# Kernel optimization log

Hardware: AMD Instinct MI355X
Metric: run time of the kernel (lower is better)

Reference implementation:

```python
import jax, jax.numpy as jnp
import numpy as np

M = 4          # num_models
B = 128        # per-model batch
C = 10         # num_classes
K = 32         # num_centroids
F = 512        # feature_dimension
NZ = 512       # noise_dimension
H = 512        # hidden_dimension
SIGMA = 1.0    # length_scale (not learnable)


def be_fc(x, W, r, s, b=None):
    # BatchEnsemble (Ensemble_orderFC): x is [M*N, in], rows ordered by model.
    N = x.shape[0] // M
    xm = x.reshape(M, N, -1) * r[:, None, :]
    out = jnp.einsum('mni,io->mno', xm, W) * s[:, None, :]
    if b is not None:
        out = out + b[:, None, :]
    return out.reshape(M * N, -1)


def setup_inputs() -> dict:
    key = jax.random.key(0)
    ks = jax.random.split(key, 16)
    sc = lambda fan_in: 1.0 / np.sqrt(fan_in)
    inp = {
        'x': jax.random.normal(ks[0], (M * B, F), dtype=jnp.float32),
        'proto_noise': jax.random.normal(ks[1], (C * K, NZ), dtype=jnp.float32),
        # layer_W: F -> F*C, bias=False
        'W_lw': jax.random.normal(ks[2], (F, F * C), dtype=jnp.float32) * sc(F),
        'r_lw': 1.0 + 0.1 * jax.random.normal(ks[3], (M, F), dtype=jnp.float32),
        's_lw': 1.0 + 0.1 * jax.random.normal(ks[4], (M, F * C), dtype=jnp.float32),
        # fc1_p: (C + NZ) -> H
        'W1': jax.random.normal(ks[5], (C + NZ, H), dtype=jnp.float32) * sc(C + NZ),
        'r1': 1.0 + 0.1 * jax.random.normal(ks[6], (M, C + NZ), dtype=jnp.float32),
        's1': 1.0 + 0.1 * jax.random.normal(ks[7], (M, H), dtype=jnp.float32),
        'b1': jnp.zeros((M, H), dtype=jnp.float32),
        # fc2_p: H -> F
        'W2': jax.random.normal(ks[8], (H, F), dtype=jnp.float32) * sc(H),
        'r2': 1.0 + 0.1 * jax.random.normal(ks[9], (M, H), dtype=jnp.float32),
        's2': 1.0 + 0.1 * jax.random.normal(ks[10], (M, F), dtype=jnp.float32),
        'b2': jnp.zeros((M, F), dtype=jnp.float32),
    }
    return inp


def reference(x, proto_noise, W_lw, r_lw, s_lw, W1, r1, s1, b1, W2, r2, s2, b2):
    # ---- get_prototype ----
    onehot = jnp.repeat(jnp.eye(C, dtype=x.dtype), K, axis=0)        # [C*K, C]
    proto_in = jnp.concatenate([proto_noise, onehot], axis=1)        # [C*K, NZ+C]
    proto_in = jnp.tile(proto_in, (M, 1))                            # [M*C*K, NZ+C]
    h = jax.nn.relu(be_fc(proto_in, W1, r1, s1, b1))
    proto = be_fc(h, W2, r2, s2, b2).reshape(M, C, K, F)

    # ---- last_layer ----
    z = be_fc(x, W_lw, r_lw, s_lw)                                   # [M*B, F*C]
    z = z.reshape(M * B, F, C)

    # ---- output_layer: broadcast RBF squared-distance reduction ----
    zt = jnp.transpose(z.reshape(M, B, F, C), (0, 1, 3, 2))          # [M, B, C, F]
    diff = zt[:, :, :, None, :] - proto[:, None, :, :, :]            # [M, B, C, K, F]
    distances = -(diff ** 2).mean(axis=(-1, -2)) / (2.0 * SIGMA ** 2)  # [M, B, C]

    logit = distances.reshape(-1, C)                                 # [M*B, C]
    return jnp.exp(logit)
```

## Files before the change

### kernel.cpp

```cpp
#include <hip/hip_runtime.h>
#include <math.h>

#define MM 4
#define BB 128
#define CC 10
#define KK 32
#define FF 512
#define HH 512
#define NP 320
#define OUTW 5120

using bf16x8 = __attribute__((ext_vector_type(8))) short;
using f32x4  = __attribute__((ext_vector_type(4))) float;

__device__ __forceinline__ unsigned short f2bf(float f) {
    unsigned int u = __float_as_uint(f);
    u += 0x7FFFu + ((u >> 16) & 1u);
    return (unsigned short)(u >> 16);
}

template<int EPI, int ASRC, int BSRC, int WR, int WC, int I, int J,
         int KSTEPS, int KREALB, int RPM, int NCOLS>
__device__ __forceinline__ void gemm_tile(
    const int bx, const int by,
    const unsigned short* __restrict__ Abf, const float* __restrict__ Af32,
    const float* __restrict__ ascale,
    const unsigned short* __restrict__ Btbf, const float* __restrict__ Bf32,
    const float* __restrict__ s, const float* __restrict__ bias,
    const float* __restrict__ auxr, void* __restrict__ outv,
    float* __restrict__ auxw, unsigned short* smem)
{
    constexpr int TR = WR * I * 16;
    constexpr int TC = WC * J * 16;
    constexpr int BUFE = (TR + TC) * 32;
    const int t = threadIdx.x;
    const int lane = t & 63;
    const int w = t >> 6;
    const int wr = w / WC, wc = w % WC;
    const int l15 = lane & 15, l4 = lane >> 4;
    const int rowT = by * TR, colT = bx * TC;
    const int m = rowT / RPM;

    constexpr bool AGUARD = (TR * 4 < 256);
    const bool aact = !AGUARD || (t < TR * 4);
    const int asrow = t >> 2, ag = t & 3;
    const int stA = asrow * 32 + ((ag ^ ((asrow >> 1) & 3)) * 8);
    const unsigned short* gA = nullptr;
    const float* gAf = nullptr;
    const float* scp = nullptr;
    int cn = 0;
    if constexpr (ASRC == 0) {
        if (aact) gA = Abf + (size_t)(rowT + asrow) * 512 + ag * 8;
    } else {
        gAf = Af32 + (size_t)((rowT % NP) + asrow) * 512 + ag * 8;
        scp = ascale + (size_t)m * 522 + ag * 8;
        cn = ((rowT % NP) + asrow) >> 5;
    }
    const int bsrow = t >> 2, bg = t & 3;
    const int stB0 = bsrow * 32 + ((bg ^ ((bsrow >> 1) & 3)) * 8);
    const int bcol = t & 63, bkg = t >> 6;
    const int stB1 = bcol * 32 + ((bkg ^ ((bcol >> 1) & 3)) * 8);
    const unsigned short* gB = nullptr;
    if constexpr (BSRC == 0)
        gB = Btbf + (size_t)(colT + bsrow) * 512 + bg * 8;

    int offA[I], offB[J];
#pragma unroll
    for (int i = 0; i < I; ++i) {
        int rA = wr * (I * 16) + i * 16 + l15;
        offA[i] = rA * 32 + ((l4 ^ ((rA >> 1) & 3)) * 8);
    }
#pragma unroll
    for (int j = 0; j < J; ++j) {
        int rB = wc * (J * 16) + j * 16 + l15;
        offB[j] = rB * 32 + ((l4 ^ ((rB >> 1) & 3)) * 8);
    }

    f32x4 acc[I][J];
#pragma unroll
    for (int i = 0; i < I; ++i)
#pragma unroll
        for (int j = 0; j < J; ++j) acc[i][j] = (f32x4){0.f, 0.f, 0.f, 0.f};

    uint4 ra, rb;
    float4 nf0, nf1, ns0, ns1;
    float rbf[8];

#define FETCH(KS)                                                              \
    {                                                                          \
        const int k0 = (KS) * 32;                                              \
        if constexpr (ASRC == 0) {                                             \
            if (aact) ra = *(const uint4*)(gA + k0);                           \
        } else {                                                               \
            if (k0 < 512) {                                                    \
                nf0 = *(const float4*)(gAf + k0);                              \
                nf1 = *(const float4*)(gAf + k0 + 4);                          \
                ns0 = *(const float4*)(scp + k0);                              \
                ns1 = *(const float4*)(scp + k0 + 4);                          \
            }                                                                  \
        }                                                                      \
        if constexpr (BSRC == 0) {                                             \
            rb = *(const uint4*)(gB + k0);                                     \
        } else {                                                               \
            _Pragma("unroll")                                                  \
            for (int q = 0; q < 8; ++q) {                                      \
                int gk = k0 + bkg * 8 + q;                                     \
                rbf[q] = (gk < KREALB)                                         \
                    ? Bf32[(size_t)gk * NCOLS + colT + bcol] : 0.f;            \
            }                                                                  \
        }                                                                      \
    }

#define WRITE(KS, BUF)                                                         \
    {                                                                          \
        const int k0 = (KS) * 32;                                              \
        unsigned short* As_ = smem + (BUF) * BUFE;                             \
        unsigned short* Bs_ = As_ + TR * 32;                                   \
        if constexpr (ASRC == 0) {                                             \
            if (aact) *(uint4*)(As_ + stA) = ra;                               \
        } else {                                                               \
            union { unsigned short u[8]; uint4 q; } o;                         \
            if (k0 < 512) {                                                    \
                float vv[8] = {nf0.x, nf0.y, nf0.z, nf0.w,                     \
                               nf1.x, nf1.y, nf1.z, nf1.w};                    \
                float ss[8] = {ns0.x, ns0.y, ns0.z, ns0.w,                     \
                               ns1.x, ns1.y, ns1.z, ns1.w};                    \
                _Pragma("unroll")                                              \
                for (int q = 0; q < 8; ++q) o.u[q] = f2bf(vv[q] * ss[q]);      \
            } else {                                                           \
                _Pragma("unroll")                                              \
                for (int q = 0; q < 8; ++q) {                                  \
                    int gk = k0 + ag * 8 + q;                                  \
                    float v = (gk < 522 && (gk - 512) == cn)                   \
                        ? ascale[(size_t)m * 522 + gk] : 0.f;                  \
                    o.u[q] = f2bf(v);                                          \
                }                                                              \
            }                                                                  \
            *(uint4*)(As_ + stA) = o.q;                                        \
        }                                                                      \
        if constexpr (BSRC == 0) {                                             \
            *(uint4*)(Bs_ + stB0) = rb;                                        \
        } else {                                                               \
            union { unsigned short u[8]; uint4 q; } o;                         \
            _Pragma("unroll")                                                  \
            for (int q = 0; q < 8; ++q) o.u[q] = f2bf(rbf[q]);                 \
            *(uint4*)(Bs_ + stB1) = o.q;                                       \
        }                                                                      \
    }

    FETCH(0);
    WRITE(0, 0);
    __syncthreads();

#pragma unroll 1
    for (int ks = 0; ks < KSTEPS; ++ks) {
        const int cur = ks & 1;
        if (ks + 1 < KSTEPS) FETCH(ks + 1);
        const unsigned short* As_ = smem + cur * BUFE;
        const unsigned short* Bs_ = As_ + TR * 32;
        bf16x8 af[I], bfv[J];
#pragma unroll
        for (int i = 0; i < I; ++i) af[i] = *(const bf16x8*)(As_ + offA[i]);
#pragma unroll
        for (int j = 0; j < J; ++j) bfv[j] = *(const bf16x8*)(Bs_ + offB[j]);
#pragma unroll
        for (int i = 0; i < I; ++i)
#pragma unroll
            for (int j = 0; j < J; ++j)
                acc[i][j] = __builtin_amdgcn_mfma_f32_16x16x32_bf16(
                    af[i], bfv[j], acc[i][j], 0, 0, 0);
        if (ks + 1 < KSTEPS) {
            WRITE(ks + 1, cur ^ 1);
            __syncthreads();
        }
    }
#undef FETCH
#undef WRITE

    if constexpr (EPI == 0) {
#pragma unroll
        for (int j = 0; j < J; ++j) {
            const int col = colT + wc * (J * 16) + j * 16 + l15;
            const float sv = s[(size_t)m * NCOLS + col];
            const float bv = bias[(size_t)m * NCOLS + col];
            const float rv = auxr[(size_t)m * NCOLS + col];
#pragma unroll
            for (int i = 0; i < I; ++i)
#pragma unroll
                for (int ir = 0; ir < 4; ++ir) {
                    const int row = rowT + wr * (I * 16) + i * 16 + l4 * 4 + ir;
                    float v = fmaxf(acc[i][j][ir] * sv + bv, 0.f) * rv;
                    ((unsigned short*)outv)[(size_t)row * NCOLS + col] = f2bf(v);
                }
        }
    } else if constexpr (EPI == 1) {
        static_assert(WR == 1 && I == 2 && J == 1, "EPI1 geometry");
        const int mq = rowT / NP;
        const int c = (rowT % NP) / KK;
        const int mc = mq * CC + c;
        const int col = colT + wc * 16 + l15;
        const float sv = s[(size_t)mq * NCOLS + col];
        const float bv = bias[(size_t)mq * NCOLS + col];
        float cs = 0.f, sq = 0.f;
#pragma unroll
        for (int i = 0; i < I; ++i)
#pragma unroll
            for (int ir = 0; ir < 4; ++ir) {
                float v = acc[i][0][ir] * sv + bv;
                cs += v;
                sq += v * v;
            }
        cs += __shfl_xor(cs, 16, 64);
        cs += __shfl_xor(cs, 32, 64);
        if (l4 == 0) ((float*)outv)[(size_t)mc * FF + col] = cs;
#pragma unroll
        for (int off = 1; off < 64; off <<= 1) sq += __shfl_xor(sq, off, 64);
        if (lane == 0) auxw[mc * 32 + bx * 4 + w] = sq;
    } else {
        static_assert(WR == 2 && WC == 2 && I == 2 && J == 2, "EPI2 geometry");
        const int cb = colT >> 9;
        const int slot = ((bx & 7) << 1) | wc;
        float sv[J], pv[J];
#pragma unroll
        for (int j = 0; j < J; ++j) {
            const int col = colT + wc * (J * 16) + j * 16 + l15;
            sv[j] = s[(size_t)m * NCOLS + (col & 511) * 10 + (col >> 9)];
            pv[j] = bias[(size_t)m * NCOLS + col];
        }
        float* dst = (float*)outv;
#pragma unroll
        for (int i = 0; i < I; ++i)
#pragma unroll
            for (int ir = 0; ir < 4; ++ir) {
                const int row = rowT + wr * (I * 16) + i * 16 + l4 * 4 + ir;
                float znv = 0.f, crv = 0.f;
#pragma unroll
                for (int j = 0; j < J; ++j) {
                    float v = acc[i][j][ir] * sv[j];
                    znv += v * v;
                    crv += v * pv[j];
                }
#pragma unroll
                for (int off = 1; off < 16; off <<= 1) {
                    znv += __shfl_xor(znv, off, 64);
                    crv += __shfl_xor(crv, off, 64);
                }
                if (l15 == 0) {
                    float2 o = {znv, crv};
                    *(float2*)(dst + ((size_t)(row * CC + cb) * 16 + slot) * 2) = o;
                }
            }
    }
}

__global__ __launch_bounds__(256) void k_phase1(
    const float* __restrict__ noise, const float* __restrict__ r1,
    const float* __restrict__ W1, const float* __restrict__ s1,
    const float* __restrict__ b1, const float* __restrict__ r2,
    const float* __restrict__ W_lw, const float* __restrict__ x,
    const float* __restrict__ r_lw,
    unsigned short* __restrict__ A2, unsigned short* __restrict__ Wlwt,
    unsigned short* __restrict__ xr)
{
    __shared__ __align__(16) unsigned short smem[8192];
    const int b = blockIdx.x;
    const int t = threadIdx.x;
    if (b < 160) {
        gemm_tile<0, 2, 1, 2, 2, 2, 2, 17, 522, NP, HH>(
            b % 8, b / 8, nullptr, noise, r1, nullptr, W1,
            s1, b1, r2, (void*)A2, nullptr, smem);
    } else if (b < 800) {
        unsigned short (*T)[65] = (unsigned short (*)[65])smem;
        const int bb = b - 160;
        const int n0 = (bb % 80) * 64, k0 = (bb / 80) * 64;
#pragma unroll
        for (int p = 0; p < 4; ++p) {
            int kk = (t >> 4) + p * 16;
            int nn = (t & 15) * 4;
            float4 v = *(const float4*)(W_lw + (size_t)(k0 + kk) * OUTW + n0 + nn);
            T[nn + 0][kk] = f2bf(v.x);
            T[nn + 1][kk] = f2bf(v.y);
            T[nn + 2][kk] = f2bf(v.z);
            T[nn + 3][kk] = f2bf(v.w);
        }
        __syncthreads();
#pragma unroll
        for (int p = 0; p < 2; ++p) {
            int n = (t >> 3) + p * 32;
            int kg = t & 7;
            union { unsigned short u[8]; uint4 v; } o;
#pragma unroll
            for (int q = 0; q < 8; ++q) o.u[q] = T[n][kg * 8 + q];
            int gn = n0 + n;
            int dr = (gn % 10) * 512 + gn / 10;
            *(uint4*)(Wlwt + (size_t)dr * 512 + k0 + kg * 8) = o.v;
        }
    } else {
        const int id = (b - 800) * 256 + t;
        const int row = id >> 6, g = id & 63;
        const int mq = row >> 7;
        const float* xp = x + (size_t)row * 512 + g * 8;
        const float* rp = r_lw + (size_t)mq * 512 + g * 8;
        union { unsigned short u[8]; uint4 v; } o;
#pragma unroll
        for (int q = 0; q < 8; ++q) o.u[q] = f2bf(xp[q] * rp[q]);
        *(uint4*)(xr + (size_t)row * 512 + g * 8) = o.v;
    }
}

__global__ __launch_bounds__(256) void k_phase2(
    const unsigned short* __restrict__ A2, const float* __restrict__ W2,
    const float* __restrict__ s2, const float* __restrict__ b2,
    float* __restrict__ psum, float* __restrict__ pn_part)
{
    __shared__ __align__(16) unsigned short smem[6144];
    gemm_tile<1, 0, 1, 1, 4, 2, 1, 16, 512, NP, FF>(
        blockIdx.x, blockIdx.y, A2, nullptr, nullptr, nullptr, W2,
        s2, b2, nullptr, (void*)psum, pn_part, smem);
}

__global__ __launch_bounds__(256) void k_phase3(
    const unsigned short* __restrict__ xr, const unsigned short* __restrict__ Wlwt,
    const float* __restrict__ s_lw, const float* __restrict__ psum,
    float* __restrict__ dist_part)
{
    __shared__ __align__(16) unsigned short smem[8192];
    gemm_tile<2, 0, 0, 2, 2, 2, 2, 16, 512, BB, OUTW>(
        blockIdx.x, blockIdx.y, xr, nullptr, nullptr, Wlwt, nullptr,
        s_lw, psum, nullptr, (void*)dist_part, nullptr, smem);
}

__global__ __launch_bounds__(256) void k_out(
    const float* __restrict__ dist_part, const float* __restrict__ pn_part,
    float* __restrict__ out)
{
    const int id = blockIdx.x * 256 + threadIdx.x;
    const int c = id % 10;
    const int mb = id / 10;
    const int mc = (mb >> 7) * 10 + c;
    const float* dp = dist_part + (size_t)id * 32;
    float zn = 0.f, cr = 0.f;
#pragma unroll
    for (int q = 0; q < 16; ++q) {
        zn += dp[q * 2];
        cr += dp[q * 2 + 1];
    }
    float pnv = 0.f;
#pragma unroll
    for (int q = 0; q < 32; ++q) pnv += pn_part[mc * 32 + q];
    const float inv = 1.f / (2.f * (float)KK * (float)FF);
    out[id] = expf(-((float)KK * zn - 2.f * cr + pnv) * inv);
}

extern "C" void kernel_launch(void* const* d_in, const int* in_sizes, int n_in,
                              void* d_out, int out_size, void* d_ws, size_t ws_size,
                              hipStream_t stream) {
    const float* x     = (const float*)d_in[0];
    const float* noise = (const float*)d_in[1];
    const float* W_lw  = (const float*)d_in[2];
    const float* r_lw  = (const float*)d_in[3];
    const float* s_lw  = (const float*)d_in[4];
    const float* W1    = (const float*)d_in[5];
    const float* r1    = (const float*)d_in[6];
    const float* s1    = (const float*)d_in[7];
    const float* b1    = (const float*)d_in[8];
    const float* W2    = (const float*)d_in[9];
    const float* r2    = (const float*)d_in[10];
    const float* s2    = (const float*)d_in[11];
    const float* b2    = (const float*)d_in[12];
    float* out = (float*)d_out;

    char* base = (char*)d_ws;
    float* psum          = (float*)(base + 0);
    float* pn_part       = (float*)(base + 81920);
    float* dist_part     = (float*)(base + 87040);
    unsigned short* A2   = (unsigned short*)(base + 742400);
    unsigned short* xr   = (unsigned short*)(base + 2053120);
    unsigned short* Wlwt = (unsigned short*)(base + 2577408);

    k_phase1<<<928, 256, 0, stream>>>(noise, r1, W1, s1, b1, r2, W_lw, x, r_lw,
                                      A2, Wlwt, xr);
    k_phase2<<<dim3(8, 40), 256, 0, stream>>>(A2, W2, s2, b2, psum, pn_part);
    k_phase3<<<dim3(80, 8), 256, 0, stream>>>(xr, Wlwt, s_lw, psum, dist_part);
    k_out<<<20, 256, 0, stream>>>(dist_part, pn_part, out);
}
```

Baseline: 56.16 us.

## Stage W_lw directly in GEMM, register double-buffer, fuse output reduction via ticket

Drops the separate W_lw transpose/bf16 pre-pass in phase1 and instead loads fp32 W_lw columns directly in phase3's B staging with in-register conversion. Phase3 gets a larger 128-row tile, a two-deep register prefetch, and an epilogue that reorders columns through shared memory to emit per-column-block partials. The separate output kernel is folded into phase3 through an atomic ticket and spin-wait by trailing blocks, which saves a launch. The trade-offs are uncoalesced strided fp32 B loads, and a spin-wait that can deadlock if the waiting blocks become resident before the producer blocks.

```diff
diff --git a/kernel.cpp b/kernel.cpp
--- a/kernel.cpp
+++ b/kernel.cpp
@@ -19,20 +19,22 @@
     return (unsigned short)(u >> 16);
 }
 
-template<int EPI, int ASRC, int BSRC, int WR, int WC, int I, int J,
+template<int EPI, int ASRC, int WR, int WC, int I, int J,
          int KSTEPS, int KREALB, int RPM, int NCOLS>
 __device__ __forceinline__ void gemm_tile(
     const int bx, const int by,
     const unsigned short* __restrict__ Abf, const float* __restrict__ Af32,
-    const float* __restrict__ ascale,
-    const unsigned short* __restrict__ Btbf, const float* __restrict__ Bf32,
+    const float* __restrict__ ascale, const float* __restrict__ Bf32,
     const float* __restrict__ s, const float* __restrict__ bias,
     const float* __restrict__ auxr, void* __restrict__ outv,
     float* __restrict__ auxw, unsigned short* smem)
 {
     constexpr int TR = WR * I * 16;
     constexpr int TC = WC * J * 16;
+    static_assert(TC == 64, "direct B staging needs TC==64");
     constexpr int BUFE = (TR + TC) * 32;
+    constexpr int NUA = (TR * 4 + 255) / 256;
+
     const int t = threadIdx.x;
     const int lane = t & 63;
     const int w = t >> 6;
@@ -41,38 +43,40 @@
     const int rowT = by * TR, colT = bx * TC;
     const int m = rowT / RPM;
 
-    constexpr bool AGUARD = (TR * 4 < 256);
-    const bool aact = !AGUARD || (t < TR * 4);
-    const int asrow = t >> 2, ag = t & 3;
-    const int stA = asrow * 32 + ((ag ^ ((asrow >> 1) & 3)) * 8);
-    const unsigned short* gA = nullptr;
+    int stA[NUA];
+    const unsigned short* gA[NUA];
     const float* gAf = nullptr;
     const float* scp = nullptr;
-    int cn = 0;
-    if constexpr (ASRC == 0) {
-        if (aact) gA = Abf + (size_t)(rowT + asrow) * 512 + ag * 8;
-    } else {
-        gAf = Af32 + (size_t)((rowT % NP) + asrow) * 512 + ag * 8;
-        scp = ascale + (size_t)m * 522 + ag * 8;
+    int cn = 0, ag2 = 0;
+#pragma unroll
+    for (int u = 0; u < NUA; ++u) {
+        const int eu = t + u * 256;
+        const int asrow = eu >> 2, ag = eu & 3;
+        stA[u] = asrow * 32 + ((ag ^ ((asrow >> 1) & 3)) * 8);
+        gA[u] = nullptr;
+        if constexpr (ASRC == 0) {
+            if (eu < TR * 4) gA[u] = Abf + (size_t)(rowT + asrow) * 512 + ag * 8;
+        }
+    }
+    if constexpr (ASRC == 2) {
+        static_assert(TR == 64, "ASRC2 needs TR==64");
+        const int asrow = t >> 2; ag2 = t & 3;
+        gAf = Af32 + (size_t)((rowT % NP) + asrow) * 512 + ag2 * 8;
+        scp = ascale + (size_t)m * 522 + ag2 * 8;
         cn = ((rowT % NP) + asrow) >> 5;
     }
-    const int bsrow = t >> 2, bg = t & 3;
-    const int stB0 = bsrow * 32 + ((bg ^ ((bsrow >> 1) & 3)) * 8);
     const int bcol = t & 63, bkg = t >> 6;
-    const int stB1 = bcol * 32 + ((bkg ^ ((bcol >> 1) & 3)) * 8);
-    const unsigned short* gB = nullptr;
-    if constexpr (BSRC == 0)
-        gB = Btbf + (size_t)(colT + bsrow) * 512 + bg * 8;
+    const int stB = bcol * 32 + ((bkg ^ ((bcol >> 1) & 3)) * 8);
 
     int offA[I], offB[J];
 #pragma unroll
     for (int i = 0; i < I; ++i) {
-        int rA = wr * (I * 16) + i * 16 + l15;
+        const int rA = wr * (I * 16) + i * 16 + l15;
         offA[i] = rA * 32 + ((l4 ^ ((rA >> 1) & 3)) * 8);
     }
 #pragma unroll
     for (int j = 0; j < J; ++j) {
-        int rB = wc * (J * 16) + j * 16 + l15;
+        const int rB = wc * (J * 16) + j * 16 + l15;
         offB[j] = rB * 32 + ((l4 ^ ((rB >> 1) & 3)) * 8);
     }
 
@@ -82,100 +86,111 @@
 #pragma unroll
         for (int j = 0; j < J; ++j) acc[i][j] = (f32x4){0.f, 0.f, 0.f, 0.f};
 
-    uint4 ra, rb;
-    float4 nf0, nf1, ns0, ns1;
-    float rbf[8];
-
-#define FETCH(KS)                                                              \
+    uint4 ra[2][NUA];
+    float4 nf0[2], nf1[2], ns0[2], ns1[2];
+    float rbf[2][8];
+
+#define FETCH(KS, SEL)                                                         \
     {                                                                          \
-        const int k0 = (KS) * 32;                                              \
+        const int k0_ = (KS) * 32;                                             \
         if constexpr (ASRC == 0) {                                             \
-            if (aact) ra = *(const uint4*)(gA + k0);                           \
+            _Pragma("unroll")                                                  \
+            for (int u = 0; u < NUA; ++u)                                      \
+                if ((t + u * 256) < TR * 4)                                    \
+                    ra[SEL][u] = *(const uint4*)(gA[u] + k0_);                 \
         } else {                                                               \
-            if (k0 < 512) {                                                    \
-                nf0 = *(const float4*)(gAf + k0);                              \
-                nf1 = *(const float4*)(gAf + k0 + 4);                          \
-                ns0 = *(const float4*)(scp + k0);                              \
-                ns1 = *(const float4*)(scp + k0 + 4);                          \
+            if (k0_ < 512) {                                                   \
+                nf0[SEL] = *(const float4*)(gAf + k0_);                        \
+                nf1[SEL] = *(const float4*)(gAf + k0_ + 4);                    \
+                ns0[SEL] = *(const float4*)(scp + k0_);                        \
+                ns1[SEL] = *(const float4*)(scp + k0_ + 4);                    \
             }                                                                  \
         }                                                                      \
-        if constexpr (BSRC == 0) {                                             \
-            rb = *(const uint4*)(gB + k0);                                     \
-        } else {                                                               \
-            _Pragma("unroll")                                                  \
-            for (int q = 0; q < 8; ++q) {                                      \
-                int gk = k0 + bkg * 8 + q;                                     \
-                rbf[q] = (gk < KREALB)                                         \
-                    ? Bf32[(size_t)gk * NCOLS + colT + bcol] : 0.f;            \
-            }                                                                  \
+        _Pragma("unroll")                                                      \
+        for (int q = 0; q < 8; ++q) {                                          \
+            const int gk = k0_ + bkg * 8 + q;                                  \
+            rbf[SEL][q] = (gk < KREALB)                                        \
+                ? Bf32[(size_t)gk * NCOLS + colT + bcol] : 0.f;                \
         }                                                                      \
     }
 
-#define WRITE(KS, BUF)                                                         \
+#define WRITE(KS, SEL, BUF)                                                    \
     {                                                                          \
-        const int k0 = (KS) * 32;                                              \
+        const int k0_ = (KS) * 32;                                             \
         unsigned short* As_ = smem + (BUF) * BUFE;                             \
         unsigned short* Bs_ = As_ + TR * 32;                                   \
         if constexpr (ASRC == 0) {                                             \
-            if (aact) *(uint4*)(As_ + stA) = ra;                               \
+            _Pragma("unroll")                                                  \
+            for (int u = 0; u < NUA; ++u)                                      \
+                if ((t + u * 256) < TR * 4) *(uint4*)(As_ + stA[u]) = ra[SEL][u]; \
         } else {                                                               \
-            union { unsigned short u[8]; uint4 q; } o;                         \
-            if (k0 < 512) {                                                    \
-                float vv[8] = {nf0.x, nf0.y, nf0.z, nf0.w,                     \
-                               nf1.x, nf1.y, nf1.z, nf1.w};                    \
-                float ss[8] = {ns0.x, ns0.y, ns0.z, ns0.w,                     \
-                               ns1.x, ns1.y, ns1.z, ns1.w};                    \
+            union { unsigned short us[8]; uint4 q4; } o;                       \
+            if (k0_ < 512) {                                                   \
+                float vv[8] = {nf0[SEL].x, nf0[SEL].y, nf0[SEL].z, nf0[SEL].w, \
+                               nf1[SEL].x, nf1[SEL].y, nf1[SEL].z, nf1[SEL].w};\
+                float ss[8] = {ns0[SEL].x, ns0[SEL].y, ns0[SEL].z, ns0[SEL].w, \
+                               ns1[SEL].x, ns1[SEL].y, ns1[SEL].z, ns1[SEL].w};\
                 _Pragma("unroll")                                              \
-                for (int q = 0; q < 8; ++q) o.u[q] = f2bf(vv[q] * ss[q]);      \
+                for (int q = 0; q < 8; ++q) o.us[q] = f2bf(vv[q] * ss[q]);     \
             } else {                                                           \
                 _Pragma("unroll")                                              \
                 for (int q = 0; q < 8; ++q) {                                  \
-                    int gk = k0 + ag * 8 + q;                                  \
+                    const int gk = k0_ + ag2 * 8 + q;                          \
                     float v = (gk < 522 && (gk - 512) == cn)                   \
                         ? ascale[(size_t)m * 522 + gk] : 0.f;                  \
-                    o.u[q] = f2bf(v);                                          \
+                    o.us[q] = f2bf(v);                                         \
                 }                                                              \
             }                                                                  \
-            *(uint4*)(As_ + stA) = o.q;                                        \
+            *(uint4*)(As_ + stA[0]) = o.q4;                                    \
         }                                                                      \
-        if constexpr (BSRC == 0) {                                             \
-            *(uint4*)(Bs_ + stB0) = rb;                                        \
-        } else {                                                               \
-            union { unsigned short u[8]; uint4 q; } o;                         \
+        {                                                                      \
+            union { unsigned short us[8]; uint4 q4; } ob;                      \
             _Pragma("unroll")                                                  \
-            for (int q = 0; q < 8; ++q) o.u[q] = f2bf(rbf[q]);                 \
-            *(uint4*)(Bs_ + stB1) = o.q;                                       \
+            for (int q = 0; q < 8; ++q) ob.us[q] = f2bf(rbf[SEL][q]);          \
+            *(uint4*)(Bs_ + stB) = ob.q4;                                      \
         }                                                                      \
     }
 
-    FETCH(0);
-    WRITE(0, 0);
+#define MFMA_STEP(BUF)                                                         \
+    {                                                                          \
+        const unsigned short* As_ = smem + (BUF) * BUFE;                       \
+        const unsigned short* Bs_ = As_ + TR * 32;                             \
+        bf16x8 af[I], bfv[J];                                                  \
+        _Pragma("unroll")                                                      \
+        for (int i = 0; i < I; ++i) af[i] = *(const bf16x8*)(As_ + offA[i]);   \
+        _Pragma("unroll")                                                      \
+        for (int j = 0; j < J; ++j) bfv[j] = *(const bf16x8*)(Bs_ + offB[j]);  \
+        _Pragma("unroll")                                                      \
+        for (int i = 0; i < I; ++i)                                            \
+            _Pragma("unroll")                                                  \
+            for (int j = 0; j < J; ++j)                                        \
+                acc[i][j] = __builtin_amdgcn_mfma_f32_16x16x32_bf16(           \
+                    af[i], bfv[j], acc[i][j], 0, 0, 0);                        \
+    }
+
+    FETCH(0, 0);
+    WRITE(0, 0, 0);
+    FETCH(1, 1);
     __syncthreads();
 
 #pragma unroll 1
-    for (int ks = 0; ks < KSTEPS; ++ks) {
-        const int cur = ks & 1;
-        if (ks + 1 < KSTEPS) FETCH(ks + 1);
-        const unsigned short* As_ = smem + cur * BUFE;
-        const unsigned short* Bs_ = As_ + TR * 32;
-        bf16x8 af[I], bfv[J];
-#pragma unroll
-        for (int i = 0; i < I; ++i) af[i] = *(const bf16x8*)(As_ + offA[i]);
-#pragma unroll
-        for (int j = 0; j < J; ++j) bfv[j] = *(const bf16x8*)(Bs_ + offB[j]);
-#pragma unroll
-        for (int i = 0; i < I; ++i)
-#pragma unroll
-            for (int j = 0; j < J; ++j)
-                acc[i][j] = __builtin_amdgcn_mfma_f32_16x16x32_bf16(
-                    af[i], bfv[j], acc[i][j], 0, 0, 0);
-        if (ks + 1 < KSTEPS) {
-            WRITE(ks + 1, cur ^ 1);
+    for (int ks2 = 0; ks2 < KSTEPS; ks2 += 2) {
+        if (ks2 + 2 < KSTEPS) FETCH(ks2 + 2, 0);
+        MFMA_STEP(0);
+        if (ks2 + 1 < KSTEPS) {
+            WRITE(ks2 + 1, 1, 1);
             __syncthreads();
+            if (ks2 + 3 < KSTEPS) FETCH(ks2 + 3, 1);
+            MFMA_STEP(1);
+            if (ks2 + 2 < KSTEPS) {
+                WRITE(ks2 + 2, 0, 0);
+                __syncthreads();
+            }
         }
     }
 #undef FETCH
 #undef WRITE
+#undef MFMA_STEP
 
     if constexpr (EPI == 0) {
 #pragma unroll
@@ -212,44 +227,47 @@
             }
         cs += __shfl_xor(cs, 16, 64);
         cs += __shfl_xor(cs, 32, 64);
-        if (l4 == 0) ((float*)outv)[(size_t)mc * FF + col] = cs;
+        if (l4 == 0)
+            ((float*)outv)[(size_t)mq * (CC * NCOLS) + (size_t)col * CC + c] = cs;
 #pragma unroll
         for (int off = 1; off < 64; off <<= 1) sq += __shfl_xor(sq, off, 64);
         if (lane == 0) auxw[mc * 32 + bx * 4 + w] = sq;
     } else {
-        static_assert(WR == 2 && WC == 2 && I == 2 && J == 2, "EPI2 geometry");
-        const int cb = colT >> 9;
-        const int slot = ((bx & 7) << 1) | wc;
-        float sv[J], pv[J];
-#pragma unroll
-        for (int j = 0; j < J; ++j) {
-            const int col = colT + wc * (J * 16) + j * 16 + l15;
-            sv[j] = s[(size_t)m * NCOLS + (col & 511) * 10 + (col >> 9)];
-            pv[j] = bias[(size_t)m * NCOLS + col];
-        }
-        float* dst = (float*)outv;
+        static_assert(WR == 2 && WC == 2 && J == 2, "EPI2 geometry");
+        __syncthreads();
+        float* zt = (float*)smem;
+        float* ps = zt + TR * 66;
+        float sv[J];
+#pragma unroll
+        for (int j = 0; j < J; ++j)
+            sv[j] = s[(size_t)m * NCOLS + colT + wc * (J * 16) + j * 16 + l15];
 #pragma unroll
         for (int i = 0; i < I; ++i)
 #pragma unroll
-            for (int ir = 0; ir < 4; ++ir) {
-                const int row = rowT + wr * (I * 16) + i * 16 + l4 * 4 + ir;
-                float znv = 0.f, crv = 0.f;
-#pragma unroll
-                for (int j = 0; j < J; ++j) {
-                    float v = acc[i][j][ir] * sv[j];
-                    znv += v * v;
-                    crv += v * pv[j];
+            for (int j = 0; j < J; ++j)
+#pragma unroll
+                for (int ir = 0; ir < 4; ++ir) {
+                    const int row_l = wr * (I * 16) + i * 16 + l4 * 4 + ir;
+                    const int col_l = wc * (J * 16) + j * 16 + l15;
+                    zt[row_l * 66 + col_l] = acc[i][j][ir] * sv[j];
                 }
-#pragma unroll
-                for (int off = 1; off < 16; off <<= 1) {
-                    znv += __shfl_xor(znv, off, 64);
-                    crv += __shfl_xor(crv, off, 64);
-                }
-                if (l15 == 0) {
-                    float2 o = {znv, crv};
-                    *(float2*)(dst + ((size_t)(row * CC + cb) * 16 + slot) * 2) = o;
-                }
+        if (t < 64) ps[t] = bias[(size_t)m * NCOLS + colT + t];
+        __syncthreads();
+        const int c0 = colT % 10;
+#pragma unroll 1
+        for (int p = t; p < TR * 10; p += 256) {
+            const int row_l = p / 10, c = p % 10;
+            int cl = c - c0; if (cl < 0) cl += 10;
+            float zn = 0.f, cr = 0.f;
+            for (; cl < 64; cl += 10) {
+                const float v = zt[row_l * 66 + cl];
+                zn += v * v;
+                cr += v * ps[cl];
             }
+            float2 o = {zn, cr};
+            *(float2*)((float*)outv +
+                ((size_t)bx * 5120 + (size_t)(rowT + row_l) * 10 + c) * 2) = o;
+        }
     }
 }
 
@@ -257,54 +275,28 @@
     const float* __restrict__ noise, const float* __restrict__ r1,
     const float* __restrict__ W1, const float* __restrict__ s1,
     const float* __restrict__ b1, const float* __restrict__ r2,
-    const float* __restrict__ W_lw, const float* __restrict__ x,
-    const float* __restrict__ r_lw,
-    unsigned short* __restrict__ A2, unsigned short* __restrict__ Wlwt,
-    unsigned short* __restrict__ xr)
+    const float* __restrict__ x, const float* __restrict__ r_lw,
+    unsigned short* __restrict__ A2, unsigned short* __restrict__ xr,
+    unsigned int* __restrict__ ticket)
 {
     __shared__ __align__(16) unsigned short smem[8192];
     const int b = blockIdx.x;
     const int t = threadIdx.x;
     if (b < 160) {
-        gemm_tile<0, 2, 1, 2, 2, 2, 2, 17, 522, NP, HH>(
-            b % 8, b / 8, nullptr, noise, r1, nullptr, W1,
+        gemm_tile<0, 2, 2, 2, 2, 2, 17, 522, NP, HH>(
+            b % 8, b / 8, nullptr, noise, r1, W1,
             s1, b1, r2, (void*)A2, nullptr, smem);
-    } else if (b < 800) {
-        unsigned short (*T)[65] = (unsigned short (*)[65])smem;
-        const int bb = b - 160;
-        const int n0 = (bb % 80) * 64, k0 = (bb / 80) * 64;
-#pragma unroll
-        for (int p = 0; p < 4; ++p) {
-            int kk = (t >> 4) + p * 16;
-            int nn = (t & 15) * 4;
-            float4 v = *(const float4*)(W_lw + (size_t)(k0 + kk) * OUTW + n0 + nn);
-            T[nn + 0][kk] = f2bf(v.x);
-            T[nn + 1][kk] = f2bf(v.y);
-            T[nn + 2][kk] = f2bf(v.z);
-            T[nn + 3][kk] = f2bf(v.w);
-        }
-        __syncthreads();
-#pragma unroll
-        for (int p = 0; p < 2; ++p) {
-            int n = (t >> 3) + p * 32;
-            int kg = t & 7;
-            union { unsigned short u[8]; uint4 v; } o;
-#pragma unroll
-            for (int q = 0; q < 8; ++q) o.u[q] = T[n][kg * 8 + q];
-            int gn = n0 + n;
-            int dr = (gn % 10) * 512 + gn / 10;
-            *(uint4*)(Wlwt + (size_t)dr * 512 + k0 + kg * 8) = o.v;
-        }
     } else {
-        const int id = (b - 800) * 256 + t;
+        const int id = (b - 160) * 256 + t;
         const int row = id >> 6, g = id & 63;
         const int mq = row >> 7;
         const float* xp = x + (size_t)row * 512 + g * 8;
         const float* rp = r_lw + (size_t)mq * 512 + g * 8;
-        union { unsigned short u[8]; uint4 v; } o;
-#pragma unroll
-        for (int q = 0; q < 8; ++q) o.u[q] = f2bf(xp[q] * rp[q]);
+        union { unsigned short us[8]; uint4 v; } o;
+#pragma unroll
+        for (int q = 0; q < 8; ++q) o.us[q] = f2bf(xp[q] * rp[q]);
         *(uint4*)(xr + (size_t)row * 512 + g * 8) = o.v;
+        if (b == 287 && t == 0) *ticket = 0u;
     }
 }
 
@@ -314,42 +306,54 @@
     float* __restrict__ psum, float* __restrict__ pn_part)
 {
     __shared__ __align__(16) unsigned short smem[6144];
-    gemm_tile<1, 0, 1, 1, 4, 2, 1, 16, 512, NP, FF>(
-        blockIdx.x, blockIdx.y, A2, nullptr, nullptr, nullptr, W2,
+    gemm_tile<1, 0, 1, 4, 2, 1, 16, 512, NP, FF>(
+        blockIdx.x, blockIdx.y, A2, nullptr, nullptr, W2,
         s2, b2, nullptr, (void*)psum, pn_part, smem);
 }
 
 __global__ __launch_bounds__(256) void k_phase3(
-    const unsigned short* __restrict__ xr, const unsigned short* __restrict__ Wlwt,
+    const unsigned short* __restrict__ xr, const float* __restrict__ W_lw,
     const float* __restrict__ s_lw, const float* __restrict__ psum,
-    float* __restrict__ dist_part)
+    float* __restrict__ dist_part, const float* __restrict__ pn_part,
+    unsigned int* __restrict__ ticket, float* __restrict__ out)
 {
-    __shared__ __align__(16) unsigned short smem[8192];
-    gemm_tile<2, 0, 0, 2, 2, 2, 2, 16, 512, BB, OUTW>(
-        blockIdx.x, blockIdx.y, xr, nullptr, nullptr, Wlwt, nullptr,
-        s_lw, psum, nullptr, (void*)dist_part, nullptr, smem);
-}
-
-__global__ __launch_bounds__(256) void k_out(
-    const float* __restrict__ dist_part, const float* __restrict__ pn_part,
-    float* __restrict__ out)
-{
-    const int id = blockIdx.x * 256 + threadIdx.x;
-    const int c = id % 10;
-    const int mb = id / 10;
-    const int mc = (mb >> 7) * 10 + c;
-    const float* dp = dist_part + (size_t)id * 32;
-    float zn = 0.f, cr = 0.f;
-#pragma unroll
-    for (int q = 0; q < 16; ++q) {
-        zn += dp[q * 2];
-        cr += dp[q * 2 + 1];
-    }
-    float pnv = 0.f;
-#pragma unroll
-    for (int q = 0; q < 32; ++q) pnv += pn_part[mc * 32 + q];
-    const float inv = 1.f / (2.f * (float)KK * (float)FF);
-    out[id] = expf(-((float)KK * zn - 2.f * cr + pnv) * inv);
+    __shared__ __align__(16) unsigned short smem[17024];
+    const int blk = blockIdx.x;
+    const int t = threadIdx.x;
+    if (blk < 320) {
+        gemm_tile<2, 0, 2, 2, 4, 2, 16, 512, BB, OUTW>(
+            blk % 80, blk / 80, xr, nullptr, nullptr, W_lw,
+            s_lw, psum, nullptr, (void*)dist_part, nullptr, smem);
+        __syncthreads();
+        if (t == 0) {
+            __threadfence();
+            __hip_atomic_fetch_add(ticket, 1u, __ATOMIC_RELEASE,
+                                   __HIP_MEMORY_SCOPE_AGENT);
+        }
+    } else {
+        if (t == 0) {
+            while (__hip_atomic_load(ticket, __ATOMIC_ACQUIRE,
+                                     __HIP_MEMORY_SCOPE_AGENT) < 320u)
+                __builtin_amdgcn_s_sleep(8);
+        }
+        __syncthreads();
+        __threadfence();
+        const int id = (blk - 320) * 256 + t;
+        const int c = id % 10;
+        const int mc = ((id / 10) >> 7) * 10 + c;
+        float zn = 0.f, cr = 0.f;
+#pragma unroll 1
+        for (int q = 0; q < 80; ++q) {
+            const float* dp = dist_part + ((size_t)q * 5120 + id) * 2;
+            zn += __hip_atomic_load(dp, __ATOMIC_RELAXED, __HIP_MEMORY_SCOPE_AGENT);
+            cr += __hip_atomic_load(dp + 1, __ATOMIC_RELAXED, __HIP_MEMORY_SCOPE_AGENT);
+        }
+        float pnv = 0.f;
+#pragma unroll
+        for (int q = 0; q < 32; ++q) pnv += pn_part[mc * 32 + q];
+        const float inv = 1.f / (2.f * (float)KK * (float)FF);
+        out[id] = expf(-((float)KK * zn - 2.f * cr + pnv) * inv);
+    }
 }
 
 extern "C" void kernel_launch(void* const* d_in, const int* in_sizes, int n_in,
@@ -374,13 +378,13 @@
     float* psum          = (float*)(base + 0);
     float* pn_part       = (float*)(base + 81920);
     float* dist_part     = (float*)(base + 87040);
-    unsigned short* A2   = (unsigned short*)(base + 742400);
-    unsigned short* xr   = (unsigned short*)(base + 2053120);
-    unsigned short* Wlwt = (unsigned short*)(base + 2577408);
-
-    k_phase1<<<928, 256, 0, stream>>>(noise, r1, W1, s1, b1, r2, W_lw, x, r_lw,
-                                      A2, Wlwt, xr);
+    unsigned int* ticket = (unsigned int*)(base + 3363840);
+    unsigned short* A2   = (unsigned short*)(base + 3364096);
+    unsigned short* xr   = (unsigned short*)(base + 4674816);
+
+    k_phase1<<<288, 256, 0, stream>>>(noise, r1, W1, s1, b1, r2, x, r_lw,
+                                      A2, xr, ticket);
     k_phase2<<<dim3(8, 40), 256, 0, stream>>>(A2, W2, s2, b2, psum, pn_part);
-    k_phase3<<<dim3(80, 8), 256, 0, stream>>>(xr, Wlwt, s_lw, psum, dist_part);
-    k_out<<<20, 256, 0, stream>>>(dist_part, pn_part, out);
-}
+    k_phase3<<<340, 256, 0, stream>>>(xr, W_lw, s_lw, psum, dist_part,
+                                      pn_part, ticket, out);
+}
```

New measurement: 126.4 us. 125% more time.

## Fuse phase2, phase3 and output into one kernel with ticket-based dependencies

Applied to the files above, without the earlier changes.

Merges the prototype GEMM, the last-layer distance GEMM and the final exp reduction into a single launch. Inter-stage ordering is enforced with global atomic tickets and spin-waits instead of kernel boundaries, so phase3 blocks do their main loop concurrently and only wait before the epilogue that reads psum. It also moves the one-hot K-extension of the first GEMM into an epilogue additive term, dropping the 17th K-step. This removes two launch gaps and tail idle time, but relies on all producer blocks being scheduled before spinning consumers, which risks deadlock or stalls on occupancy.

```diff
diff --git a/kernel.cpp b/kernel.cpp
--- a/kernel.cpp
+++ b/kernel.cpp
@@ -20,7 +20,7 @@
 }
 
 template<int EPI, int ASRC, int BSRC, int WR, int WC, int I, int J,
-         int KSTEPS, int KREALB, int RPM, int NCOLS>
+         int KSTEPS, int RPM, int NCOLS>
 __device__ __forceinline__ void gemm_tile(
     const int bx, const int by,
     const unsigned short* __restrict__ Abf, const float* __restrict__ Af32,
@@ -28,10 +28,14 @@
     const unsigned short* __restrict__ Btbf, const float* __restrict__ Bf32,
     const float* __restrict__ s, const float* __restrict__ bias,
     const float* __restrict__ auxr, void* __restrict__ outv,
-    float* __restrict__ auxw, unsigned short* smem)
+    float* __restrict__ auxw,
+    const float* __restrict__ ohW, const float* __restrict__ ohR,
+    unsigned int* dep_ticket, unsigned int dep_count,
+    unsigned short* smem)
 {
     constexpr int TR = WR * I * 16;
     constexpr int TC = WC * J * 16;
+    static_assert(TR <= 64 && TC == 64, "staging geometry");
     constexpr int BUFE = (TR + TC) * 32;
     const int t = threadIdx.x;
     const int lane = t & 63;
@@ -48,13 +52,12 @@
     const unsigned short* gA = nullptr;
     const float* gAf = nullptr;
     const float* scp = nullptr;
-    int cn = 0;
     if constexpr (ASRC == 0) {
         if (aact) gA = Abf + (size_t)(rowT + asrow) * 512 + ag * 8;
     } else {
+        static_assert(TR == 64, "ASRC2 needs TR==64");
         gAf = Af32 + (size_t)((rowT % NP) + asrow) * 512 + ag * 8;
         scp = ascale + (size_t)m * 522 + ag * 8;
-        cn = ((rowT % NP) + asrow) >> 5;
     }
     const int bsrow = t >> 2, bg = t & 3;
     const int stB0 = bsrow * 32 + ((bg ^ ((bsrow >> 1) & 3)) * 8);
@@ -67,12 +70,12 @@
     int offA[I], offB[J];
 #pragma unroll
     for (int i = 0; i < I; ++i) {
-        int rA = wr * (I * 16) + i * 16 + l15;
+        const int rA = wr * (I * 16) + i * 16 + l15;
         offA[i] = rA * 32 + ((l4 ^ ((rA >> 1) & 3)) * 8);
     }
 #pragma unroll
     for (int j = 0; j < J; ++j) {
-        int rB = wc * (J * 16) + j * 16 + l15;
+        const int rB = wc * (J * 16) + j * 16 + l15;
         offB[j] = rB * 32 + ((l4 ^ ((rB >> 1) & 3)) * 8);
     }
 
@@ -88,63 +91,49 @@
 
 #define FETCH(KS)                                                              \
     {                                                                          \
-        const int k0 = (KS) * 32;                                              \
+        const int k0_ = (KS) * 32;                                             \
         if constexpr (ASRC == 0) {                                             \
-            if (aact) ra = *(const uint4*)(gA + k0);                           \
+            if (aact) ra = *(const uint4*)(gA + k0_);                          \
         } else {                                                               \
-            if (k0 < 512) {                                                    \
-                nf0 = *(const float4*)(gAf + k0);                              \
-                nf1 = *(const float4*)(gAf + k0 + 4);                          \
-                ns0 = *(const float4*)(scp + k0);                              \
-                ns1 = *(const float4*)(scp + k0 + 4);                          \
-            }                                                                  \
+            nf0 = *(const float4*)(gAf + k0_);                                 \
+            nf1 = *(const float4*)(gAf + k0_ + 4);                             \
+            ns0 = *(const float4*)(scp + k0_);                                 \
+            ns1 = *(const float4*)(scp + k0_ + 4);                             \
         }                                                                      \
         if constexpr (BSRC == 0) {                                             \
-            rb = *(const uint4*)(gB + k0);                                     \
+            rb = *(const uint4*)(gB + k0_);                                    \
         } else {                                                               \
             _Pragma("unroll")                                                  \
             for (int q = 0; q < 8; ++q) {                                      \
-                int gk = k0 + bkg * 8 + q;                                     \
-                rbf[q] = (gk < KREALB)                                         \
-                    ? Bf32[(size_t)gk * NCOLS + colT + bcol] : 0.f;            \
+                const int gk = k0_ + bkg * 8 + q;                              \
+                rbf[q] = Bf32[(size_t)gk * NCOLS + colT + bcol];               \
             }                                                                  \
         }                                                                      \
     }
 
 #define WRITE(KS, BUF)                                                         \
     {                                                                          \
-        const int k0 = (KS) * 32;                                              \
         unsigned short* As_ = smem + (BUF) * BUFE;                             \
         unsigned short* Bs_ = As_ + TR * 32;                                   \
         if constexpr (ASRC == 0) {                                             \
             if (aact) *(uint4*)(As_ + stA) = ra;                               \
         } else {                                                               \
-            union { unsigned short u[8]; uint4 q; } o;                         \
-            if (k0 < 512) {                                                    \
-                float vv[8] = {nf0.x, nf0.y, nf0.z, nf0.w,                     \
-                               nf1.x, nf1.y, nf1.z, nf1.w};                    \
-                float ss[8] = {ns0.x, ns0.y, ns0.z, ns0.w,                     \
-                               ns1.x, ns1.y, ns1.z, ns1.w};                    \
-                _Pragma("unroll")                                              \
-                for (int q = 0; q < 8; ++q) o.u[q] = f2bf(vv[q] * ss[q]);      \
-            } else {                                                           \
-                _Pragma("unroll")                                              \
-                for (int q = 0; q < 8; ++q) {                                  \
-                    int gk = k0 + ag * 8 + q;                                  \
-                    float v = (gk < 522 && (gk - 512) == cn)                   \
-                        ? ascale[(size_t)m * 522 + gk] : 0.f;                  \
-                    o.u[q] = f2bf(v);                                          \
-                }                                                              \
-            }                                                                  \
-            *(uint4*)(As_ + stA) = o.q;                                        \
+            union { unsigned short us[8]; uint4 q4; } o;                       \
+            float vv[8] = {nf0.x, nf0.y, nf0.z, nf0.w,                         \
+                           nf1.x, nf1.y, nf1.z, nf1.w};                        \
+            float ss[8] = {ns0.x, ns0.y, ns0.z, ns0.w,                         \
+                           ns1.x, ns1.y, ns1.z, ns1.w};                        \
+            _Pragma("unroll")                                                  \
+            for (int q = 0; q < 8; ++q) o.us[q] = f2bf(vv[q] * ss[q]);         \
+            *(uint4*)(As_ + stA) = o.q4;                                       \
         }                                                                      \
         if constexpr (BSRC == 0) {                                             \
             *(uint4*)(Bs_ + stB0) = rb;                                        \
         } else {                                                               \
-            union { unsigned short u[8]; uint4 q; } o;                         \
+            union { unsigned short us[8]; uint4 q4; } ob;                      \
             _Pragma("unroll")                                                  \
-            for (int q = 0; q < 8; ++q) o.u[q] = f2bf(rbf[q]);                 \
-            *(uint4*)(Bs_ + stB1) = o.q;                                       \
+            for (int q = 0; q < 8; ++q) ob.us[q] = f2bf(rbf[q]);               \
+            *(uint4*)(Bs_ + stB1) = ob.q4;                                     \
         }                                                                      \
     }
 
@@ -189,7 +178,10 @@
 #pragma unroll
                 for (int ir = 0; ir < 4; ++ir) {
                     const int row = rowT + wr * (I * 16) + i * 16 + l4 * 4 + ir;
-                    float v = fmaxf(acc[i][j][ir] * sv + bv, 0.f) * rv;
+                    const int cn = (row % NP) >> 5;
+                    const float term = ohR[(size_t)m * 522 + 512 + cn] *
+                                       ohW[(size_t)(512 + cn) * NCOLS + col];
+                    float v = fmaxf((acc[i][j][ir] + term) * sv + bv, 0.f) * rv;
                     ((unsigned short*)outv)[(size_t)row * NCOLS + col] = f2bf(v);
                 }
         }
@@ -217,7 +209,16 @@
         for (int off = 1; off < 64; off <<= 1) sq += __shfl_xor(sq, off, 64);
         if (lane == 0) auxw[mc * 32 + bx * 4 + w] = sq;
     } else {
-        static_assert(WR == 2 && WC == 2 && I == 2 && J == 2, "EPI2 geometry");
+        static_assert(WR == 2 && WC == 2 && J == 2, "EPI2 geometry");
+        if (dep_ticket != nullptr) {
+            __syncthreads();
+            if (t == 0) {
+                while (__hip_atomic_load(dep_ticket, __ATOMIC_ACQUIRE,
+                                         __HIP_MEMORY_SCOPE_AGENT) < dep_count)
+                    __builtin_amdgcn_s_sleep(2);
+            }
+            __syncthreads();
+        }
         const int cb = colT >> 9;
         const int slot = ((bx & 7) << 1) | wc;
         float sv[J], pv[J];
@@ -225,7 +226,8 @@
         for (int j = 0; j < J; ++j) {
             const int col = colT + wc * (J * 16) + j * 16 + l15;
             sv[j] = s[(size_t)m * NCOLS + (col & 511) * 10 + (col >> 9)];
-            pv[j] = bias[(size_t)m * NCOLS + col];
+            pv[j] = __hip_atomic_load((float*)&bias[(size_t)m * NCOLS + col],
+                                      __ATOMIC_RELAXED, __HIP_MEMORY_SCOPE_AGENT);
         }
         float* dst = (float*)outv;
 #pragma unroll
@@ -260,15 +262,15 @@
     const float* __restrict__ W_lw, const float* __restrict__ x,
     const float* __restrict__ r_lw,
     unsigned short* __restrict__ A2, unsigned short* __restrict__ Wlwt,
-    unsigned short* __restrict__ xr)
+    unsigned short* __restrict__ xr, unsigned int* __restrict__ tickets)
 {
     __shared__ __align__(16) unsigned short smem[8192];
     const int b = blockIdx.x;
     const int t = threadIdx.x;
     if (b < 160) {
-        gemm_tile<0, 2, 1, 2, 2, 2, 2, 17, 522, NP, HH>(
+        gemm_tile<0, 2, 1, 2, 2, 2, 2, 16, NP, HH>(
             b % 8, b / 8, nullptr, noise, r1, nullptr, W1,
-            s1, b1, r2, (void*)A2, nullptr, smem);
+            s1, b1, r2, (void*)A2, nullptr, W1, r1, nullptr, 0u, smem);
     } else if (b < 800) {
         unsigned short (*T)[65] = (unsigned short (*)[65])smem;
         const int bb = b - 160;
@@ -288,9 +290,9 @@
         for (int p = 0; p < 2; ++p) {
             int n = (t >> 3) + p * 32;
             int kg = t & 7;
-            union { unsigned short u[8]; uint4 v; } o;
-#pragma unroll
-            for (int q = 0; q < 8; ++q) o.u[q] = T[n][kg * 8 + q];
+            union { unsigned short us[8]; uint4 v; } o;
+#pragma unroll
+            for (int q = 0; q < 8; ++q) o.us[q] = T[n][kg * 8 + q];
             int gn = n0 + n;
             int dr = (gn % 10) * 512 + gn / 10;
             *(uint4*)(Wlwt + (size_t)dr * 512 + k0 + kg * 8) = o.v;
@@ -301,55 +303,76 @@
         const int mq = row >> 7;
         const float* xp = x + (size_t)row * 512 + g * 8;
         const float* rp = r_lw + (size_t)mq * 512 + g * 8;
-        union { unsigned short u[8]; uint4 v; } o;
-#pragma unroll
-        for (int q = 0; q < 8; ++q) o.u[q] = f2bf(xp[q] * rp[q]);
+        union { unsigned short us[8]; uint4 v; } o;
+#pragma unroll
+        for (int q = 0; q < 8; ++q) o.us[q] = f2bf(xp[q] * rp[q]);
         *(uint4*)(xr + (size_t)row * 512 + g * 8) = o.v;
+        if (b == 800 && t == 0) { tickets[0] = 0u; tickets[1] = 0u; }
     }
 }
 
-__global__ __launch_bounds__(256) void k_phase2(
+__global__ __launch_bounds__(256) void k_fused2(
     const unsigned short* __restrict__ A2, const float* __restrict__ W2,
     const float* __restrict__ s2, const float* __restrict__ b2,
-    float* __restrict__ psum, float* __restrict__ pn_part)
-{
-    __shared__ __align__(16) unsigned short smem[6144];
-    gemm_tile<1, 0, 1, 1, 4, 2, 1, 16, 512, NP, FF>(
-        blockIdx.x, blockIdx.y, A2, nullptr, nullptr, nullptr, W2,
-        s2, b2, nullptr, (void*)psum, pn_part, smem);
-}
-
-__global__ __launch_bounds__(256) void k_phase3(
+    float* __restrict__ psum, float* __restrict__ pn_part,
     const unsigned short* __restrict__ xr, const unsigned short* __restrict__ Wlwt,
-    const float* __restrict__ s_lw, const float* __restrict__ psum,
-    float* __restrict__ dist_part)
+    const float* __restrict__ s_lw, float* __restrict__ dist_part,
+    unsigned int* __restrict__ tickets, float* __restrict__ out)
 {
     __shared__ __align__(16) unsigned short smem[8192];
-    gemm_tile<2, 0, 0, 2, 2, 2, 2, 16, 512, BB, OUTW>(
-        blockIdx.x, blockIdx.y, xr, nullptr, nullptr, Wlwt, nullptr,
-        s_lw, psum, nullptr, (void*)dist_part, nullptr, smem);
-}
-
-__global__ __launch_bounds__(256) void k_out(
-    const float* __restrict__ dist_part, const float* __restrict__ pn_part,
-    float* __restrict__ out)
-{
-    const int id = blockIdx.x * 256 + threadIdx.x;
-    const int c = id % 10;
-    const int mb = id / 10;
-    const int mc = (mb >> 7) * 10 + c;
-    const float* dp = dist_part + (size_t)id * 32;
-    float zn = 0.f, cr = 0.f;
-#pragma unroll
-    for (int q = 0; q < 16; ++q) {
-        zn += dp[q * 2];
-        cr += dp[q * 2 + 1];
-    }
-    float pnv = 0.f;
-#pragma unroll
-    for (int q = 0; q < 32; ++q) pnv += pn_part[mc * 32 + q];
-    const float inv = 1.f / (2.f * (float)KK * (float)FF);
-    out[id] = expf(-((float)KK * zn - 2.f * cr + pnv) * inv);
+    const int blk = blockIdx.x;
+    const int t = threadIdx.x;
+    if (blk < 320) {
+        gemm_tile<1, 0, 1, 1, 4, 2, 1, 16, NP, FF>(
+            blk % 8, blk / 8, A2, nullptr, nullptr, nullptr, W2,
+            s2, b2, nullptr, (void*)psum, pn_part, nullptr, nullptr,
+            nullptr, 0u, smem);
+        __syncthreads();
+        if (t == 0) {
+            __threadfence();
+            __hip_atomic_fetch_add(&tickets[0], 1u, __ATOMIC_RELEASE,
+                                   __HIP_MEMORY_SCOPE_AGENT);
+        }
+    } else if (blk < 960) {
+        const int zb = blk - 320;
+        gemm_tile<2, 0, 0, 2, 2, 2, 2, 16, BB, OUTW>(
+            zb % 80, zb / 80, xr, nullptr, nullptr, Wlwt, nullptr,
+            s_lw, psum, nullptr, (void*)dist_part, nullptr, nullptr, nullptr,
+            &tickets[0], 320u, smem);
+        __syncthreads();
+        if (t == 0) {
+            __threadfence();
+            __hip_atomic_fetch_add(&tickets[1], 1u, __ATOMIC_RELEASE,
+                                   __HIP_MEMORY_SCOPE_AGENT);
+        }
+    } else {
+        if (t == 0) {
+            while (__hip_atomic_load(&tickets[1], __ATOMIC_ACQUIRE,
+                                     __HIP_MEMORY_SCOPE_AGENT) < 640u)
+                __builtin_amdgcn_s_sleep(8);
+        }
+        __syncthreads();
+        __threadfence();
+        const int id = (blk - 960) * 256 + t;
+        const int c = id % 10;
+        const int mc = ((id / 10) >> 7) * 10 + c;
+        float zn = 0.f, cr = 0.f;
+        const float* dp = dist_part + (size_t)id * 32;
+#pragma unroll
+        for (int q = 0; q < 16; ++q) {
+            zn += __hip_atomic_load((float*)&dp[q * 2], __ATOMIC_RELAXED,
+                                    __HIP_MEMORY_SCOPE_AGENT);
+            cr += __hip_atomic_load((float*)&dp[q * 2 + 1], __ATOMIC_RELAXED,
+                                    __HIP_MEMORY_SCOPE_AGENT);
+        }
+        float pnv = 0.f;
+#pragma unroll
+        for (int q = 0; q < 32; ++q)
+            pnv += __hip_atomic_load((float*)&pn_part[mc * 32 + q],
+                                     __ATOMIC_RELAXED, __HIP_MEMORY_SCOPE_AGENT);
+        const float inv = 1.f / (2.f * (float)KK * (float)FF);
+        out[id] = expf(-((float)KK * zn - 2.f * cr + pnv) * inv);
+    }
 }
 
 extern "C" void kernel_launch(void* const* d_in, const int* in_sizes, int n_in,
@@ -374,13 +397,13 @@
     float* psum          = (float*)(base + 0);
     float* pn_part       = (float*)(base + 81920);
     float* dist_part     = (float*)(base + 87040);
-    unsigned short* A2   = (unsigned short*)(base + 742400);
-    unsigned short* xr   = (unsigned short*)(base + 2053120);
-    unsigned short* Wlwt = (unsigned short*)(base + 2577408);
+    unsigned int* tickets= (unsigned int*)(base + 742400);
+    unsigned short* A2   = (unsigned short*)(base + 742656);
+    unsigned short* xr   = (unsigned short*)(base + 2053376);
+    unsigned short* Wlwt = (unsigned short*)(base + 2577664);
 
     k_phase1<<<928, 256, 0, stream>>>(noise, r1, W1, s1, b1, r2, W_lw, x, r_lw,
-                                      A2, Wlwt, xr);
-    k_phase2<<<dim3(8, 40), 256, 0, stream>>>(A2, W2, s2, b2, psum, pn_part);
-    k_phase3<<<dim3(80, 8), 256, 0, stream>>>(xr, Wlwt, s_lw, psum, dist_part);
-    k_out<<<20, 256, 0, stream>>>(dist_part, pn_part, out);
+                                      A2, Wlwt, xr, tickets);
+    k_fused2<<<980, 256, 0, stream>>>(A2, W2, s2, b2, psum, pn_part,
+                                      xr, Wlwt, s_lw, dist_part, tickets, out);
 }
```

Result: slower. 147.7 us, median of 4 (+163.1%).
